# Performance work log

Hardware: AMD Instinct MI355X
Metric: run time of the kernel (lower is better)

## Reference

```python
import jax, jax.numpy as jnp
import numpy as np


def setup_inputs() -> dict:
    key = jax.random.key(0)
    k1, k2 = jax.random.split(key)
    src_map = jax.random.normal(k1, (8, 256, 48, 48), dtype=jnp.float32)
    dst_map = jax.random.normal(k2, (8, 256, 48, 48), dtype=jnp.float32)
    return {"src_map": src_map, "dst_map": dst_map}


def reference(src_map, dst_map):
    # src_map: [B, C, H, W] -> flatten spatial to S = H*W
    B, C, H, W = src_map.shape
    src_flat = src_map.reshape(B, C, H * W)                 # [B, C, S]
    # L2-normalize along channel dim (torch.norm default: 2-norm, no eps)
    src = src_flat / jnp.linalg.norm(src_flat, axis=1, keepdims=True)
    dst = dst_map / jnp.linalg.norm(dst_map, axis=1, keepdims=True)  # [B, C, Y, X]
    # cosine correlation volume: for each src pixel s, dot with every dst pixel
    gcm = jnp.einsum('bcs,bcyx->bsyx', src, dst)            # [B, S, Y, X]
    # torch.max(gcm, 0) == ReLU clamp
    return jnp.maximum(gcm, 0.0)
```

## Files before the change

kernel.cpp:

```cpp
#include <hip/hip_runtime.h>
#include <hip/hip_bf16.h>

#define B_DIM 8
#define C_DIM 256
#define S_DIM 2304

#define ROW_STRIDE 40
#define TILE_ELEMS (128 * ROW_STRIDE)

typedef __attribute__((ext_vector_type(8))) short short8;
typedef __attribute__((ext_vector_type(4))) float floatx4;

__device__ __forceinline__ void barrier_lgkm() {
    asm volatile("s_waitcnt lgkmcnt(0)\n\ts_barrier" ::: "memory");
}

__global__ __launch_bounds__(256) void norm_transpose_kernel(
    const float* __restrict__ src, const float* __restrict__ dst,
    __hip_bfloat16* __restrict__ srcT, __hip_bfloat16* __restrict__ dstT) {
    const int s0 = blockIdx.x * 64;
    const int b  = blockIdx.y;
    const float* in = (blockIdx.z == 0 ? src : dst) + (size_t)b * C_DIM * S_DIM;
    __hip_bfloat16* out = (blockIdx.z == 0 ? srcT : dstT) + (size_t)b * S_DIM * C_DIM;

    __shared__ __align__(16) __hip_bfloat16 tile[64][C_DIM + 8];
    __shared__ float red[4][64];
    __shared__ float invn[64];

    const int t  = threadIdx.x;
    const int l  = t & 63;
    const int wv = t >> 6;

    float ss = 0.f;
#pragma unroll 8
    for (int c = wv; c < C_DIM; c += 4) {
        float v = in[(size_t)c * S_DIM + s0 + l];
        ss += v * v;
        tile[l][c] = __float2bfloat16(v);
    }
    red[wv][l] = ss;
    __syncthreads();
    if (t < 64) invn[t] = rsqrtf(red[0][t] + red[1][t] + red[2][t] + red[3][t]);
    __syncthreads();

#pragma unroll
    for (int it = 0; it < 8; ++it) {
        int idx  = it * 256 + t;
        int srow = idx >> 5;
        int c0   = (idx & 31) << 3;
        float inv = invn[srow];
        union { short8 v; __hip_bfloat16 h[8]; } u, o;
        u.v = *(const short8*)&tile[srow][c0];
#pragma unroll
        for (int j = 0; j < 8; ++j)
            o.h[j] = __float2bfloat16(__bfloat162float(u.h[j]) * inv);
        *(short8*)&out[(size_t)(s0 + srow) * C_DIM + c0] = o.v;
    }
}

__global__ __launch_bounds__(256) void gemm_relu_kernel(
    const __hip_bfloat16* __restrict__ At, const __hip_bfloat16* __restrict__ Bt,
    float* __restrict__ out) {
    const int id = blockIdx.x;
    const int b  = id & 7;
    const int q  = id >> 3;
    const int m0 = (q % 18) * 128;
    const int n0 = (q / 18) * 128;
    const __hip_bfloat16* A  = At + (size_t)b * S_DIM * C_DIM;
    const __hip_bfloat16* Bp = Bt + (size_t)b * S_DIM * C_DIM;

    __shared__ __align__(16) unsigned char smem[2 * 2 * TILE_ELEMS * 2];
    __hip_bfloat16* stg = (__hip_bfloat16*)smem;
    float* Cs = (float*)smem;

    const int t    = threadIdx.x;
    const int lane = t & 63;
    const int wv   = t >> 6;

    const int fm = lane & 15;
    const int kq = (lane >> 4) << 3;
    const int wr = (wv >> 1) << 6;
    const int wc = (wv & 1) << 6;
    const int rq = (lane >> 4) << 2;

    const int e0   = wv * 1024 + lane * 8;
    const int row0 = e0 >> 5, kc0 = e0 & 31;
    const int e1   = e0 + 512;
    const int row1 = e1 >> 5, kc1 = e1 & 31;
    const int p0 = row0 * ROW_STRIDE + kc0;
    const int p1 = row1 * ROW_STRIDE + kc1;

    const __hip_bfloat16* gA0 = A  + (size_t)(m0 + row0) * C_DIM + kc0;
    const __hip_bfloat16* gA1 = A  + (size_t)(m0 + row1) * C_DIM + kc1;
    const __hip_bfloat16* gB0 = Bp + (size_t)(n0 + row0) * C_DIM + kc0;
    const __hip_bfloat16* gB1 = Bp + (size_t)(n0 + row1) * C_DIM + kc1;

    short8 rA0 = *(const short8*)gA0;
    short8 rA1 = *(const short8*)gA1;
    short8 rB0 = *(const short8*)gB0;
    short8 rB1 = *(const short8*)gB1;

    floatx4 acc[4][4] = {};

#pragma unroll
    for (int ki = 0; ki < 8; ++ki) {
        __hip_bfloat16* As = stg + (ki & 1) * TILE_ELEMS;
        __hip_bfloat16* Bs = stg + 2 * TILE_ELEMS + (ki & 1) * TILE_ELEMS;

        *(short8*)(As + p0) = rA0;
        *(short8*)(As + p1) = rA1;
        *(short8*)(Bs + p0) = rB0;
        *(short8*)(Bs + p1) = rB1;

        if (ki < 7) {
            int off = (ki + 1) * 32;
            rA0 = *(const short8*)(gA0 + off);
            rA1 = *(const short8*)(gA1 + off);
            rB0 = *(const short8*)(gB0 + off);
            rB1 = *(const short8*)(gB1 + off);
        }

        barrier_lgkm();

        short8 af[4], bf[4];
#pragma unroll
        for (int i = 0; i < 4; ++i) {
            af[i] = *(const short8*)&As[(wr + i * 16 + fm) * ROW_STRIDE + kq];
            bf[i] = *(const short8*)&Bs[(wc + i * 16 + fm) * ROW_STRIDE + kq];
        }
        __builtin_amdgcn_s_setprio(1);
#pragma unroll
        for (int i = 0; i < 4; ++i)
#pragma unroll
            for (int j = 0; j < 4; ++j)
                acc[i][j] = __builtin_amdgcn_mfma_f32_16x16x32_bf16(af[i], bf[j], acc[i][j], 0, 0, 0);
        __builtin_amdgcn_s_setprio(0);
    }

    float* Cp = out + (size_t)b * S_DIM * S_DIM;
#pragma unroll
    for (int p = 0; p < 2; ++p) {
        __syncthreads();
#pragma unroll
        for (int i2 = 0; i2 < 2; ++i2) {
            int i = 2 * p + i2;
            int slot = (wr >> 1) + i2 * 16 + rq;
#pragma unroll
            for (int j = 0; j < 4; ++j) {
                int col = wc + j * 16 + fm;
#pragma unroll
                for (int r = 0; r < 4; ++r)
                    Cs[(slot + r) * 132 + col] = fmaxf(acc[i][j][r], 0.f);
            }
        }
        __syncthreads();
#pragma unroll
        for (int it = 0; it < 8; ++it) {
            int idx  = it * 256 + t;
            int srow = idx >> 5;
            int c4   = (idx & 31) << 2;
            float4 v = *(const float4*)&Cs[srow * 132 + c4];
            int lrow = 32 * p + (srow & 31) + ((srow >> 5) << 6);
            *(float4*)&Cp[(size_t)(m0 + lrow) * S_DIM + n0 + c4] = v;
        }
    }
}

extern "C" void kernel_launch(void* const* d_in, const int* in_sizes, int n_in,
                              void* d_out, int out_size, void* d_ws, size_t ws_size,
                              hipStream_t stream) {
    const float* src = (const float*)d_in[0];
    const float* dst = (const float*)d_in[1];
    float* out = (float*)d_out;

    __hip_bfloat16* srcT = (__hip_bfloat16*)d_ws;
    __hip_bfloat16* dstT = srcT + (size_t)B_DIM * S_DIM * C_DIM;

    dim3 g1(S_DIM / 64, B_DIM, 2);
    norm_transpose_kernel<<<g1, 256, 0, stream>>>(src, dst, srcT, dstT);

    gemm_relu_kernel<<<dim3(B_DIM * 18 * 18), 256, 0, stream>>>(srcT, dstT, out);
}
```

Baseline: 209.5 us.

## Pre-swizzle operands into MFMA fragment layout and load GEMM fragments directly from global

```diff
diff --git a/kernel.cpp b/kernel.cpp
--- a/kernel.cpp
+++ b/kernel.cpp
@@ -5,15 +5,9 @@
 #define C_DIM 256
 #define S_DIM 2304
 
-#define ROW_STRIDE 40
-#define TILE_ELEMS (128 * ROW_STRIDE)
 
 typedef __attribute__((ext_vector_type(8))) short short8;
 typedef __attribute__((ext_vector_type(4))) float floatx4;
-
-__device__ __forceinline__ void barrier_lgkm() {
-    asm volatile("s_waitcnt lgkmcnt(0)\n\ts_barrier" ::: "memory");
-}
 
 __global__ __launch_bounds__(256) void norm_transpose_kernel(
     const float* __restrict__ src, const float* __restrict__ dst,
@@ -45,20 +39,22 @@
 
 #pragma unroll
     for (int it = 0; it < 8; ++it) {
-        int idx  = it * 256 + t;
-        int srow = idx >> 5;
-        int c0   = (idx & 31) << 3;
+        int gidx = it * 256 + t;
+        int fm   = gidx & 15;
+        int cg   = (gidx >> 4) & 31;
+        int sg   = gidx >> 9;
+        int srow = sg * 16 + fm;
         float inv = invn[srow];
         union { short8 v; __hip_bfloat16 h[8]; } u, o;
-        u.v = *(const short8*)&tile[srow][c0];
+        u.v = *(const short8*)&tile[srow][cg * 8];
 #pragma unroll
         for (int j = 0; j < 8; ++j)
             o.h[j] = __float2bfloat16(__bfloat162float(u.h[j]) * inv);
-        *(short8*)&out[(size_t)(s0 + srow) * C_DIM + c0] = o.v;
+        *(short8*)&out[(size_t)((s0 >> 4) + sg) * 4096 + cg * 128 + fm * 8] = o.v;
     }
 }
 
-__global__ __launch_bounds__(256) void gemm_relu_kernel(
+__global__ __launch_bounds__(256, 3) void gemm_relu_kernel(
     const __hip_bfloat16* __restrict__ At, const __hip_bfloat16* __restrict__ Bt,
     float* __restrict__ out) {
     const int id = blockIdx.x;
@@ -66,74 +62,60 @@
     const int q  = id >> 3;
     const int m0 = (q % 18) * 128;
     const int n0 = (q / 18) * 128;
-    const __hip_bfloat16* A  = At + (size_t)b * S_DIM * C_DIM;
-    const __hip_bfloat16* Bp = Bt + (size_t)b * S_DIM * C_DIM;
 
-    __shared__ __align__(16) unsigned char smem[2 * 2 * TILE_ELEMS * 2];
-    __hip_bfloat16* stg = (__hip_bfloat16*)smem;
-    float* Cs = (float*)smem;
+    __shared__ __align__(16) float Cs[64 * 132];
 
     const int t    = threadIdx.x;
     const int lane = t & 63;
     const int wv   = t >> 6;
 
     const int fm = lane & 15;
-    const int kq = (lane >> 4) << 3;
     const int wr = (wv >> 1) << 6;
     const int wc = (wv & 1) << 6;
     const int rq = (lane >> 4) << 2;
 
-    const int e0   = wv * 1024 + lane * 8;
-    const int row0 = e0 >> 5, kc0 = e0 & 31;
-    const int e1   = e0 + 512;
-    const int row1 = e1 >> 5, kc1 = e1 & 31;
-    const int p0 = row0 * ROW_STRIDE + kc0;
-    const int p1 = row1 * ROW_STRIDE + kc1;
-
-    const __hip_bfloat16* gA0 = A  + (size_t)(m0 + row0) * C_DIM + kc0;
-    const __hip_bfloat16* gA1 = A  + (size_t)(m0 + row1) * C_DIM + kc1;
-    const __hip_bfloat16* gB0 = Bp + (size_t)(n0 + row0) * C_DIM + kc0;
-    const __hip_bfloat16* gB1 = Bp + (size_t)(n0 + row1) * C_DIM + kc1;
-
-    short8 rA0 = *(const short8*)gA0;
-    short8 rA1 = *(const short8*)gA1;
-    short8 rB0 = *(const short8*)gB0;
-    short8 rB1 = *(const short8*)gB1;
+    const __hip_bfloat16* pA = At + (size_t)b * S_DIM * C_DIM
+                             + (size_t)((m0 + wr) >> 4) * 4096 + lane * 8;
+    const __hip_bfloat16* pB = Bt + (size_t)b * S_DIM * C_DIM
+                             + (size_t)((n0 + wc) >> 4) * 4096 + lane * 8;
 
     floatx4 acc[4][4] = {};
+    short8 a0[4], b0[4], a1[4], b1[4];
 
 #pragma unroll
-    for (int ki = 0; ki < 8; ++ki) {
-        __hip_bfloat16* As = stg + (ki & 1) * TILE_ELEMS;
-        __hip_bfloat16* Bs = stg + 2 * TILE_ELEMS + (ki & 1) * TILE_ELEMS;
+    for (int i = 0; i < 4; ++i) {
+        a0[i] = *(const short8*)(pA + i * 4096);
+        b0[i] = *(const short8*)(pB + i * 4096);
+    }
 
-        *(short8*)(As + p0) = rA0;
-        *(short8*)(As + p1) = rA1;
-        *(short8*)(Bs + p0) = rB0;
-        *(short8*)(Bs + p1) = rB1;
-
-        if (ki < 7) {
-            int off = (ki + 1) * 32;
-            rA0 = *(const short8*)(gA0 + off);
-            rA1 = *(const short8*)(gA1 + off);
-            rB0 = *(const short8*)(gB0 + off);
-            rB1 = *(const short8*)(gB1 + off);
-        }
-
-        barrier_lgkm();
-
-        short8 af[4], bf[4];
+#pragma unroll
+    for (int ki = 0; ki < 8; ki += 2) {
 #pragma unroll
         for (int i = 0; i < 4; ++i) {
-            af[i] = *(const short8*)&As[(wr + i * 16 + fm) * ROW_STRIDE + kq];
-            bf[i] = *(const short8*)&Bs[(wc + i * 16 + fm) * ROW_STRIDE + kq];
+            a1[i] = *(const short8*)(pA + i * 4096 + (ki + 1) * 512);
+            b1[i] = *(const short8*)(pB + i * 4096 + (ki + 1) * 512);
         }
         __builtin_amdgcn_s_setprio(1);
 #pragma unroll
         for (int i = 0; i < 4; ++i)
 #pragma unroll
             for (int j = 0; j < 4; ++j)
-                acc[i][j] = __builtin_amdgcn_mfma_f32_16x16x32_bf16(af[i], bf[j], acc[i][j], 0, 0, 0);
+                acc[i][j] = __builtin_amdgcn_mfma_f32_16x16x32_bf16(a0[i], b0[j], acc[i][j], 0, 0, 0);
+        __builtin_amdgcn_s_setprio(0);
+
+        if (ki + 2 < 8) {
+#pragma unroll
+            for (int i = 0; i < 4; ++i) {
+                a0[i] = *(const short8*)(pA + i * 4096 + (ki + 2) * 512);
+                b0[i] = *(const short8*)(pB + i * 4096 + (ki + 2) * 512);
+            }
+        }
+        __builtin_amdgcn_s_setprio(1);
+#pragma unroll
+        for (int i = 0; i < 4; ++i)
+#pragma unroll
+            for (int j = 0; j < 4; ++j)
+                acc[i][j] = __builtin_amdgcn_mfma_f32_16x16x32_bf16(a1[i], b1[j], acc[i][j], 0, 0, 0);
         __builtin_amdgcn_s_setprio(0);
     }
 
```

Result: no change. 210.4 us (+0.5%).
